# Optimization experiments

Measured on AMD Instinct MI355X. Metric: run time of the kernel, lower is better.

## Reference

```python
import jax, jax.numpy as jnp
import numpy as np

BLOCK_Q = 64
BLOCK_KV = 64
TOPK_RATIO = 0.125


def setup_inputs() -> dict:
    key = jax.random.key(0)
    k1, k2, k3 = jax.random.split(key, 3)
    B, H, L, D = 1, 16, 8192, 64
    q = jax.random.normal(k1, (B, H, L, D), dtype=jnp.float32)
    k = jax.random.normal(k2, (B, H, L, D), dtype=jnp.float32)
    v = jax.random.normal(k3, (B, H, L, D), dtype=jnp.float32)
    return {"q": q, "k": k, "v": v}


def _sparse_lut(q, k):
    # get_sparse_map: block mean-pool q and mean-centered k, score blocks, top-k key blocks
    B, H, L, D = q.shape
    Mb, Nb = L // BLOCK_Q, L // BLOCK_KV
    q_pool = q.reshape(B, H, Mb, BLOCK_Q, D).mean(axis=3)          # [B,H,Mb,D]
    smooth_k = k - k.mean(axis=-2, keepdims=True)
    k_pool = smooth_k.reshape(B, H, Nb, BLOCK_KV, D).mean(axis=3)  # [B,H,Nb,D]
    pred = jnp.einsum('bhmd,bhnd->bhmn', q_pool, k_pool)           # [B,H,Mb,Nb]
    topk = int(TOPK_RATIO * Nb)
    _, lut = jax.lax.top_k(pred, topk)                             # [B,H,Mb,topk]
    return lut


def reference(q, k, v):
    B, H, L, D = q.shape
    Mb, Nb = L // BLOCK_Q, L // BLOCK_KV
    lut = _sparse_lut(q, k)                                        # [B,H,Mb,T] int32
    T = lut.shape[-1]
    sm_scale = D ** -0.5

    kb = k.reshape(B, H, Nb, BLOCK_KV, D)
    vb = v.reshape(B, H, Nb, BLOCK_KV, D)
    bi = jnp.arange(B)[:, None, None, None]
    hi = jnp.arange(H)[None, :, None, None]
    # gather selected KV blocks per query block: [B,H,Mb,T,BLOCK_KV,D]
    k_sel = kb[bi, hi, lut].reshape(B, H, Mb, T * BLOCK_KV, D)
    v_sel = vb[bi, hi, lut].reshape(B, H, Mb, T * BLOCK_KV, D)

    qb = q.reshape(B, H, Mb, BLOCK_Q, D)
    s = jnp.einsum('bhmqd,bhmkd->bhmqk', qb, k_sel) * sm_scale     # [B,H,Mb,BQ,T*BKV]
    p = jax.nn.softmax(s, axis=-1)
    o = jnp.einsum('bhmqk,bhmkd->bhmqd', p, v_sel)
    return o.reshape(B, H, L, D)
```

## Files before the change

### kernel.cpp

```cpp
#include <hip/hip_runtime.h>
#include <hip/hip_bf16.h>


#define H_  16
#define L_  8192
#define D_  64
#define MB_ 128
#define NB_ 128
#define TK_ 16
#define ST_ 72
#define PST 80

typedef __bf16 bf16x8 __attribute__((ext_vector_type(8)));
typedef float  f32x4  __attribute__((ext_vector_type(4)));
typedef unsigned short u16x8 __attribute__((ext_vector_type(8)));

union BFU { __hip_bfloat16 h; unsigned short u; };

static __device__ inline unsigned short f2bfu(float f) {
  BFU c; c.h = __float2bfloat16(f); return c.u;
}

__device__ unsigned short g_qb[(size_t)H_ * L_ * D_];
__device__ unsigned short g_kb[(size_t)H_ * L_ * D_];
__device__ unsigned short g_vt[(size_t)H_ * D_ * L_];
__device__ float g_qpool[H_ * NB_ * 64];
__device__ float g_kpool[H_ * NB_ * 64];
__device__ int   g_lut[H_ * MB_ * TK_];

static __device__ inline void cvt8_2(const float4& f0, const float4& f1,
                                     unsigned short* dst) {
  u16x8 s;
  s[0] = f2bfu(f0.x); s[1] = f2bfu(f0.y); s[2] = f2bfu(f0.z); s[3] = f2bfu(f0.w);
  s[4] = f2bfu(f1.x); s[5] = f2bfu(f1.y); s[6] = f2bfu(f1.z); s[7] = f2bfu(f1.w);
  *(u16x8*)dst = s;
}

static __device__ inline void cvt8_2s(const float4& f0, const float4& f1,
                                      unsigned short* dst, float sc) {
  u16x8 s;
  s[0] = f2bfu(f0.x * sc); s[1] = f2bfu(f0.y * sc);
  s[2] = f2bfu(f0.z * sc); s[3] = f2bfu(f0.w * sc);
  s[4] = f2bfu(f1.x * sc); s[5] = f2bfu(f1.y * sc);
  s[6] = f2bfu(f1.z * sc); s[7] = f2bfu(f1.w * sc);
  *(u16x8*)dst = s;
}

__global__ __launch_bounds__(256)
void fusedpool_kernel(const float* __restrict__ q,
                      const float* __restrict__ k,
                      const float* __restrict__ v) {
  __shared__ float qt[64 * 64];
  __shared__ float kt[64 * 64];
  __shared__ __align__(16) unsigned short vt_s[64 * ST_];
  __shared__ float pq[4][64], pk[4][64];

  const int b = blockIdx.x;
  const int h = b >> 7, n = b & 127;
  const int t = threadIdx.x;
  const int r = t >> 2, c = (t & 3) * 16;
  const size_t base = (size_t)b * 4096 + r * 64 + c;
  const float cs = 0.18033688011112042f;

  float4 qf0 = *(const float4*)(q + base),      qf1 = *(const float4*)(q + base + 4);
  float4 qf2 = *(const float4*)(q + base + 8),  qf3 = *(const float4*)(q + base + 12);
  float4 kf0 = *(const float4*)(k + base),      kf1 = *(const float4*)(k + base + 4);
  float4 kf2 = *(const float4*)(k + base + 8),  kf3 = *(const float4*)(k + base + 12);
  float4 vf0 = *(const float4*)(v + base),      vf1 = *(const float4*)(v + base + 4);
  float4 vf2 = *(const float4*)(v + base + 8),  vf3 = *(const float4*)(v + base + 12);

  cvt8_2s(qf0, qf1, g_qb + base, cs);  cvt8_2s(qf2, qf3, g_qb + base + 8, cs);
  cvt8_2(kf0, kf1, g_kb + base);       cvt8_2(kf2, kf3, g_kb + base + 8);
  cvt8_2(vf0, vf1, vt_s + r * ST_ + c);
  cvt8_2(vf2, vf3, vt_s + r * ST_ + c + 8);

  *(float4*)(qt + r * 64 + c)      = qf0; *(float4*)(qt + r * 64 + c + 4)  = qf1;
  *(float4*)(qt + r * 64 + c + 8)  = qf2; *(float4*)(qt + r * 64 + c + 12) = qf3;
  *(float4*)(kt + r * 64 + c)      = kf0; *(float4*)(kt + r * 64 + c + 4)  = kf1;
  *(float4*)(kt + r * 64 + c + 8)  = kf2; *(float4*)(kt + r * 64 + c + 12) = kf3;
  __syncthreads();

  const int col = t & 63, g = t >> 6;
  float sq = 0.f, sk = 0.f;
  for (int rr = g * 16; rr < g * 16 + 16; ++rr) {
    sq += qt[rr * 64 + col];
    sk += kt[rr * 64 + col];
  }
  pq[g][col] = sq; pk[g][col] = sk;

  u16x8 va, vb;
  #pragma unroll
  for (int i = 0; i < 8; ++i) va[i] = vt_s[(c + i) * ST_ + r];
  #pragma unroll
  for (int i = 0; i < 8; ++i) vb[i] = vt_s[(c + 8 + i) * ST_ + r];
  const size_t vo = ((size_t)h * 64 + r) * (size_t)L_ + (size_t)n * 64 + c;
  *(u16x8*)(g_vt + vo)     = va;
  *(u16x8*)(g_vt + vo + 8) = vb;

  __syncthreads();
  if (t < 64) {
    g_qpool[b * 64 + t] = (pq[0][t] + pq[1][t] + pq[2][t] + pq[3][t]) * (1.f / 64.f);
    g_kpool[b * 64 + t] = (pk[0][t] + pk[1][t] + pk[2][t] + pk[3][t]) * (1.f / 64.f);
  }
}


__global__ void topk_kernel() {
  const int b = blockIdx.x;
  const int h = b >> 7;
  const int lane = threadIdx.x;
  const float4* qrow = (const float4*)(g_qpool + b * 64);
  const float4* k0 = (const float4*)(g_kpool + (h * NB_ + lane) * 64);
  const float4* k1 = (const float4*)(g_kpool + (h * NB_ + lane + 64) * 64);
  float v0 = 0.f, v1 = 0.f;
  for (int i = 0; i < 16; ++i) {
    float4 qv = qrow[i];
    float4 a = k0[i];
    float4 c = k1[i];
    v0 += qv.x * a.x + qv.y * a.y + qv.z * a.z + qv.w * a.w;
    v1 += qv.x * c.x + qv.y * c.y + qv.z * c.z + qv.w * c.w;
  }
  for (int t = 0; t < TK_; ++t) {
    float bv; int bi;
    if (v0 >= v1) { bv = v0; bi = lane; } else { bv = v1; bi = lane + 64; }
    for (int mask = 1; mask < 64; mask <<= 1) {
      float ov = __shfl_xor(bv, mask, 64);
      int   oi = __shfl_xor(bi, mask, 64);
      if (ov > bv || (ov == bv && oi < bi)) { bv = ov; bi = oi; }
    }
    if (lane == 0) g_lut[b * TK_ + t] = bi;
    if (bi == lane) v0 = -3.0e38f;
    else if (bi == lane + 64) v1 = -3.0e38f;
  }
}

__global__ __launch_bounds__(256, 4)
void attn_kernel(float* __restrict__ out) {
  __shared__ __align__(16) unsigned short Ks[64 * ST_];
  __shared__ __align__(16) unsigned short Vt[64 * ST_];
  __shared__ __align__(16) unsigned short Pw[4][16 * PST];

  const int blk = blockIdx.x;
  const int h = blk & 15, m = blk >> 4;
  const int t = threadIdx.x;
  const int w = t >> 6;
  const int lane = t & 63;
  const int l16 = lane & 15, quad = lane >> 4;
  const int srow = t >> 3, scol = (t & 7) * 8;
  const int vd = t >> 2, vc = (t & 3) * 16;

  const unsigned short* qg = g_qb + ((size_t)h * L_ + (size_t)m * 64) * D_;
  const unsigned short* qrow = qg + (16 * w + l16) * 64 + quad * 8;
  const bf16x8 aq0 = *(const bf16x8*)(qrow);
  const bf16x8 aq1 = *(const bf16x8*)(qrow + 32);

  f32x4 o[4];
  #pragma unroll
  for (int n4 = 0; n4 < 4; ++n4) o[n4] = (f32x4){0.f, 0.f, 0.f, 0.f};
  float lsum = 0.f;

  const int* my_lut = g_lut + (h * MB_ + m) * TK_;
  const unsigned short* vg = g_vt + (size_t)h * D_ * L_;

  const int kb0 = my_lut[0] & 127;
  const size_t koff0 = ((size_t)h * L_ + (size_t)kb0 * 64) * D_;
  u16x8 kx0 = *(const u16x8*)(g_kb + koff0 + t * 8);
  u16x8 kx1 = *(const u16x8*)(g_kb + koff0 + 2048 + t * 8);
  u16x8 vx0 = *(const u16x8*)(vg + (size_t)vd * L_ + kb0 * 64 + vc);
  u16x8 vx1 = *(const u16x8*)(vg + (size_t)vd * L_ + kb0 * 64 + vc + 8);

  for (int j = 0; j < TK_; ++j) {
    *(u16x8*)(Ks + srow * ST_ + scol)        = kx0;
    *(u16x8*)(Ks + (32 + srow) * ST_ + scol) = kx1;
    *(u16x8*)(Vt + vd * ST_ + vc)     = vx0;
    *(u16x8*)(Vt + vd * ST_ + vc + 8) = vx1;
    __syncthreads();

    if (j + 1 < TK_) {
      const int kb = my_lut[j + 1] & 127;
      const size_t koff = ((size_t)h * L_ + (size_t)kb * 64) * D_;
      kx0 = *(const u16x8*)(g_kb + koff + t * 8);
      kx1 = *(const u16x8*)(g_kb + koff + 2048 + t * 8);
      vx0 = *(const u16x8*)(vg + (size_t)vd * L_ + kb * 64 + vc);
      vx1 = *(const u16x8*)(vg + (size_t)vd * L_ + kb * 64 + vc + 8);
    }

    f32x4 acc[4];
    #pragma unroll
    for (int n4 = 0; n4 < 4; ++n4) {
      bf16x8 a0 = *(const bf16x8*)&Ks[(n4 * 16 + l16) * ST_ + quad * 8];
      bf16x8 a1 = *(const bf16x8*)&Ks[(n4 * 16 + l16) * ST_ + 32 + quad * 8];
      f32x4 z = (f32x4){0.f, 0.f, 0.f, 0.f};
      z = __builtin_amdgcn_mfma_f32_16x16x32_bf16(a0, aq0, z, 0, 0, 0);
      z = __builtin_amdgcn_mfma_f32_16x16x32_bf16(a1, aq1, z, 0, 0, 0);
      acc[n4] = z;
    }

    unsigned short* pw = &Pw[w][0];
    #pragma unroll
    for (int n4 = 0; n4 < 4; ++n4) {
      const float p0 = exp2f(acc[n4][0]), p1 = exp2f(acc[n4][1]);
      const float p2 = exp2f(acc[n4][2]), p3 = exp2f(acc[n4][3]);
      lsum += (p0 + p1) + (p2 + p3);
      unsigned int d0, d1;
      asm("v_cvt_pk_bf16_f32 %0, %1, %2" : "=v"(d0) : "v"(p0), "v"(p1));
      asm("v_cvt_pk_bf16_f32 %0, %1, %2" : "=v"(d1) : "v"(p2), "v"(p3));
      uint2 dd; dd.x = d0; dd.y = d1;
      *(uint2*)&pw[l16 * PST + n4 * 16 + quad * 4] = dd;
    }

    asm volatile("s_waitcnt lgkmcnt(0)" ::: "memory");
    __builtin_amdgcn_sched_barrier(0);

    const bf16x8 pa0 = *(const bf16x8*)&pw[l16 * PST + quad * 8];
    const bf16x8 pa1 = *(const bf16x8*)&pw[l16 * PST + 32 + quad * 8];

    #pragma unroll
    for (int n4 = 0; n4 < 4; ++n4) {
      bf16x8 v0f = *(const bf16x8*)&Vt[(n4 * 16 + l16) * ST_ + quad * 8];
      bf16x8 v1f = *(const bf16x8*)&Vt[(n4 * 16 + l16) * ST_ + 32 + quad * 8];
      o[n4] = __builtin_amdgcn_mfma_f32_16x16x32_bf16(pa0, v0f, o[n4], 0, 0, 0);
      o[n4] = __builtin_amdgcn_mfma_f32_16x16x32_bf16(pa1, v1f, o[n4], 0, 0, 0);
    }
    __syncthreads();
  }

  float rs = lsum;
  rs += __shfl_xor(rs, 16, 64);
  rs += __shfl_xor(rs, 32, 64);
  const float rinv = 1.0f / rs;
  float ri[4];
  #pragma unroll
  for (int r = 0; r < 4; ++r) ri[r] = __shfl(rinv, quad * 4 + r, 64);

  const size_t obase = ((size_t)h * L_ + (size_t)m * 64) * D_;
  #pragma unroll
  for (int n4 = 0; n4 < 4; ++n4) {
    #pragma unroll
    for (int r = 0; r < 4; ++r) {
      const int qrow_o = 16 * w + quad * 4 + r;
      out[obase + (size_t)qrow_o * 64 + n4 * 16 + l16] = o[n4][r] * ri[r];
    }
  }
}

extern "C" void kernel_launch(void* const* d_in, const int* in_sizes, int n_in,
                              void* d_out, int out_size, void* d_ws, size_t ws_size,
                              hipStream_t stream) {
  const float* q = (const float*)d_in[0];
  const float* k = (const float*)d_in[1];
  const float* v = (const float*)d_in[2];
  float* out = (float*)d_out;

  fusedpool_kernel<<<H_ * NB_, 256, 0, stream>>>(q, k, v);
  topk_kernel<<<H_ * MB_, 64, 0, stream>>>();
  attn_kernel<<<H_ * MB_, 256, 0, stream>>>(out);
}
```

Baseline: 235.7 us.

## Double-buffer K/V shared tiles and drop the trailing per-iteration barrier

Splits the K and V shared-memory tiles into two buffers alternating by iteration, which lets the end-of-loop __syncthreads be removed so each iteration has one barrier instead of two. It also issues the next block's global loads before the barrier, reads the LUT index through readfirstlane so addressing is scalar, raises wave priority around the MFMA sections, and narrows the P-tile stride from 80 to 72. The costs are more LDS per block, which could reduce occupancy, and possible LDS bank-conflict changes from the new stride.

```diff
diff --git a/kernel.cpp b/kernel.cpp
--- a/kernel.cpp
+++ b/kernel.cpp
@@ -9,7 +9,7 @@
 #define NB_ 128
 #define TK_ 16
 #define ST_ 72
-#define PST 80
+#define PST 72
 
 typedef __bf16 bf16x8 __attribute__((ext_vector_type(8)));
 typedef float  f32x4  __attribute__((ext_vector_type(4)));
@@ -136,8 +136,8 @@
 
 __global__ __launch_bounds__(256, 4)
 void attn_kernel(float* __restrict__ out) {
-  __shared__ __align__(16) unsigned short Ks[64 * ST_];
-  __shared__ __align__(16) unsigned short Vt[64 * ST_];
+  __shared__ __align__(16) unsigned short Ks[2][64 * ST_];
+  __shared__ __align__(16) unsigned short Vt[2][64 * ST_];
   __shared__ __align__(16) unsigned short Pw[4][16 * PST];
 
   const int blk = blockIdx.x;
@@ -160,41 +160,44 @@
   float lsum = 0.f;
 
   const int* my_lut = g_lut + (h * MB_ + m) * TK_;
+  const unsigned short* kh = g_kb + (size_t)h * L_ * D_;
   const unsigned short* vg = g_vt + (size_t)h * D_ * L_;
 
-  const int kb0 = my_lut[0] & 127;
-  const size_t koff0 = ((size_t)h * L_ + (size_t)kb0 * 64) * D_;
-  u16x8 kx0 = *(const u16x8*)(g_kb + koff0 + t * 8);
-  u16x8 kx1 = *(const u16x8*)(g_kb + koff0 + 2048 + t * 8);
-  u16x8 vx0 = *(const u16x8*)(vg + (size_t)vd * L_ + kb0 * 64 + vc);
-  u16x8 vx1 = *(const u16x8*)(vg + (size_t)vd * L_ + kb0 * 64 + vc + 8);
+  int kb = __builtin_amdgcn_readfirstlane(my_lut[0]);
+  u16x8 kx0 = *(const u16x8*)(kh + kb * 4096 + t * 8);
+  u16x8 kx1 = *(const u16x8*)(kh + kb * 4096 + 2048 + t * 8);
+  u16x8 vx0 = *(const u16x8*)(vg + (size_t)vd * L_ + kb * 64 + vc);
+  u16x8 vx1 = *(const u16x8*)(vg + (size_t)vd * L_ + kb * 64 + vc + 8);
 
   for (int j = 0; j < TK_; ++j) {
-    *(u16x8*)(Ks + srow * ST_ + scol)        = kx0;
-    *(u16x8*)(Ks + (32 + srow) * ST_ + scol) = kx1;
-    *(u16x8*)(Vt + vd * ST_ + vc)     = vx0;
-    *(u16x8*)(Vt + vd * ST_ + vc + 8) = vx1;
+    const int buf = j & 1;
+    *(u16x8*)(Ks[buf] + srow * ST_ + scol)        = kx0;
+    *(u16x8*)(Ks[buf] + (32 + srow) * ST_ + scol) = kx1;
+    *(u16x8*)(Vt[buf] + vd * ST_ + vc)     = vx0;
+    *(u16x8*)(Vt[buf] + vd * ST_ + vc + 8) = vx1;
+
+    if (j + 1 < TK_) {
+      const int kbn = __builtin_amdgcn_readfirstlane(my_lut[j + 1]);
+      kx0 = *(const u16x8*)(kh + kbn * 4096 + t * 8);
+      kx1 = *(const u16x8*)(kh + kbn * 4096 + 2048 + t * 8);
+      vx0 = *(const u16x8*)(vg + (size_t)vd * L_ + kbn * 64 + vc);
+      vx1 = *(const u16x8*)(vg + (size_t)vd * L_ + kbn * 64 + vc + 8);
+    }
+
     __syncthreads();
 
-    if (j + 1 < TK_) {
-      const int kb = my_lut[j + 1] & 127;
-      const size_t koff = ((size_t)h * L_ + (size_t)kb * 64) * D_;
-      kx0 = *(const u16x8*)(g_kb + koff + t * 8);
-      kx1 = *(const u16x8*)(g_kb + koff + 2048 + t * 8);
-      vx0 = *(const u16x8*)(vg + (size_t)vd * L_ + kb * 64 + vc);
-      vx1 = *(const u16x8*)(vg + (size_t)vd * L_ + kb * 64 + vc + 8);
-    }
-
     f32x4 acc[4];
+    __builtin_amdgcn_s_setprio(1);
     #pragma unroll
     for (int n4 = 0; n4 < 4; ++n4) {
-      bf16x8 a0 = *(const bf16x8*)&Ks[(n4 * 16 + l16) * ST_ + quad * 8];
-      bf16x8 a1 = *(const bf16x8*)&Ks[(n4 * 16 + l16) * ST_ + 32 + quad * 8];
+      bf16x8 a0 = *(const bf16x8*)&Ks[buf][(n4 * 16 + l16) * ST_ + quad * 8];
+      bf16x8 a1 = *(const bf16x8*)&Ks[buf][(n4 * 16 + l16) * ST_ + 32 + quad * 8];
       f32x4 z = (f32x4){0.f, 0.f, 0.f, 0.f};
       z = __builtin_amdgcn_mfma_f32_16x16x32_bf16(a0, aq0, z, 0, 0, 0);
       z = __builtin_amdgcn_mfma_f32_16x16x32_bf16(a1, aq1, z, 0, 0, 0);
       acc[n4] = z;
     }
+    __builtin_amdgcn_s_setprio(0);
 
     unsigned short* pw = &Pw[w][0];
     #pragma unroll
@@ -215,14 +218,15 @@
     const bf16x8 pa0 = *(const bf16x8*)&pw[l16 * PST + quad * 8];
     const bf16x8 pa1 = *(const bf16x8*)&pw[l16 * PST + 32 + quad * 8];
 
+    __builtin_amdgcn_s_setprio(1);
     #pragma unroll
     for (int n4 = 0; n4 < 4; ++n4) {
-      bf16x8 v0f = *(const bf16x8*)&Vt[(n4 * 16 + l16) * ST_ + quad * 8];
-      bf16x8 v1f = *(const bf16x8*)&Vt[(n4 * 16 + l16) * ST_ + 32 + quad * 8];
+      bf16x8 v0f = *(const bf16x8*)&Vt[buf][(n4 * 16 + l16) * ST_ + quad * 8];
+      bf16x8 v1f = *(const bf16x8*)&Vt[buf][(n4 * 16 + l16) * ST_ + 32 + quad * 8];
       o[n4] = __builtin_amdgcn_mfma_f32_16x16x32_bf16(pa0, v0f, o[n4], 0, 0, 0);
       o[n4] = __builtin_amdgcn_mfma_f32_16x16x32_bf16(pa1, v1f, o[n4], 0, 0, 0);
     }
-    __syncthreads();
+    __builtin_amdgcn_s_setprio(0);
   }
 
   float rs = lsum;
```

New measurement: 236.3 us. About the same (+0.2%).
